# Kernel tuning notes

Measured on AMD Instinct MI355X. Metric: run time of the kernel, lower is better.

Reference implementation:

```python
import jax, jax.numpy as jnp
import numpy as np
import math

D = 256   # d_model / hidden_size
Q = 256   # q_num (query-side nodes)
K = 512   # k_num (key-side nodes)
NEG = -9e15


def _forward(q_enc, k_enc, rel_k, rel_v, k_adj,
             W_glob, b_glob, W_gv0, b_gv0, W_gv1, b_gv1,
             W_gq, b_gq, W_lq, b_lq,
             W_locgate, b_locgate, W_gate, b_gate):
    d = q_enc.shape[-1]
    scale = 1.0 / math.sqrt(d)
    act = jnp.tanh  # activation_func='tanh'

    # --- global sigmoid blending of k_enc with the mean query encoding ---
    q_glob_enc = jnp.mean(q_enc, axis=0)                       # [d]
    k_s = jax.nn.sigmoid((q_glob_enc @ W_glob + b_glob) @ k_enc.T * scale)  # [K]
    k_s = k_s[:, None]                                         # [K,1]
    g_1 = q_glob_enc @ W_gv0 + b_gv0                           # [d]
    k_1 = k_enc @ W_gv1 + b_gv1                                # [K,d]
    k_enc2 = (1.0 - k_s) * k_1 + k_s * g_1                     # [K,d]

    # --- global relation-aware attention over k nodes ---
    q_glob = q_enc @ W_gq + b_gq                               # [Q,d]
    qk_logit = q_glob @ k_enc2.T                               # [Q,K]
    qk_r = jnp.einsum('qd,qkd->qk', q_glob, rel_k)             # [Q,K]
    glob_attn = jax.nn.softmax(act((qk_logit + qk_r) * scale), axis=-1)  # [Q,K]

    # --- local adjacency-masked attention ---
    q_loc = q_enc @ W_lq + b_lq                                # [Q,d]
    qnk_logit = q_loc @ k_enc2.T                               # [Q,K]
    qnk_r = jnp.einsum('qd,qkd->qk', q_loc, rel_k)             # [Q,K]
    loc_attn = act((qnk_logit + qnk_r) * scale)                # [Q,K]
    # loc_weight_rep[q,i,j] = loc_attn[q,j]  (repeat + view in torch)
    mask = (k_adj != 0)[None, :, :]                            # [1,K,K]
    masked = jnp.where(mask, loc_attn[:, None, :], NEG)        # [Q,K,K]
    attn_adj_norm = jax.nn.softmax(masked, axis=-1)            # [Q,K,K]
    k_loc = jnp.einsum('qij,jd->qid', attn_adj_norm, k_enc2)   # [Q,K,d]

    # --- local gate between neighborhood value and self value ---
    # sigmoid(cat([k_loc, k_self]) @ W_locgate + b); k_self is broadcast k_enc2
    Wg1, Wg2 = W_locgate[:d], W_locgate[d:]                    # [d,1] each
    gate_logit = (jnp.einsum('qid,d->qi', k_loc, Wg1[:, 0])
                  + (k_enc2 @ Wg2)[None, :, 0] + b_locgate[0])  # [Q,K]
    loc_gate = jax.nn.sigmoid(gate_logit)[..., None]           # [Q,K,1]
    k_awr = loc_gate * k_loc + (1.0 - loc_gate) * k_enc2[None, :, :]  # [Q,K,d]

    # --- aggregate with global attention + relation values ---
    k_matmul = jnp.einsum('qk,qkd->qd', glob_attn, k_awr)      # [Q,d]
    k_r_matmul = jnp.einsum('qk,qkd->qd', glob_attn, rel_v)    # [Q,d]
    q_enc_new = k_matmul + k_r_matmul                          # [Q,d]

    # --- residual gate ---
    Wq1, Wq2 = W_gate[:d], W_gate[d:]
    gate = jax.nn.sigmoid(q_enc_new @ Wq1 + q_enc @ Wq2 + b_gate)  # [Q,1]
    h = gate * q_enc_new + (1.0 - gate) * q_enc                # [Q,d]
    return h


def setup_inputs() -> dict:
    key = jax.random.key(0)
    ks = jax.random.split(key, 16)
    def w(k, shape):
        return jax.random.normal(k, shape, jnp.float32) * 0.02
    return {
        'q_enc': jax.random.normal(ks[0], (Q, D), jnp.float32),
        'k_enc': jax.random.normal(ks[1], (K, D), jnp.float32),
        'rel_k': jax.random.normal(ks[2], (Q, K, D), jnp.float32) * 0.1,
        'rel_v': jax.random.normal(ks[3], (Q, K, D), jnp.float32) * 0.1,
        'k_adj': jax.random.randint(ks[4], (K, K), 0, 2, jnp.int64) if jax.config.jax_enable_x64 else jax.random.randint(ks[4], (K, K), 0, 2, jnp.int32),
        'W_glob': w(ks[5], (D, D)), 'b_glob': jnp.zeros((D,), jnp.float32),
        'W_gv0': w(ks[6], (D, D)), 'b_gv0': jnp.zeros((D,), jnp.float32),
        'W_gv1': w(ks[7], (D, D)), 'b_gv1': jnp.zeros((D,), jnp.float32),
        'W_gq': w(ks[8], (D, D)), 'b_gq': jnp.zeros((D,), jnp.float32),
        'W_lq': w(ks[9], (D, D)), 'b_lq': jnp.zeros((D,), jnp.float32),
        'W_locgate': w(ks[10], (2 * D, 1)), 'b_locgate': jnp.zeros((1,), jnp.float32),
        'W_gate': w(ks[11], (2 * D, 1)), 'b_gate': jnp.zeros((1,), jnp.float32),
    }


def reference(q_enc, k_enc, rel_k, rel_v, k_adj,
              W_glob, b_glob, W_gv0, b_gv0, W_gv1, b_gv1,
              W_gq, b_gq, W_lq, b_lq,
              W_locgate, b_locgate, W_gate, b_gate):
    return _forward(q_enc, k_enc, rel_k, rel_v, k_adj,
                    W_glob, b_glob, W_gv0, b_gv0, W_gv1, b_gv1,
                    W_gq, b_gq, W_lq, b_lq,
                    W_locgate, b_locgate, W_gate, b_gate)
```

## Files before the change

### kernel.cpp

```cpp
#include <hip/hip_runtime.h>
#include <math.h>

#define QN 256
#define KN 512
#define DN 256
#define SCALE 0.0625f

typedef __attribute__((ext_vector_type(8))) short short8v;
typedef __attribute__((ext_vector_type(4))) float f32x4;

__device__ __forceinline__ float sigf(float x){ return 1.0f/(1.0f+expf(-x)); }

__device__ __forceinline__ unsigned short f2bf(float x){
  unsigned u = __float_as_uint(x);
  unsigned r = (u + 0x7FFFu + ((u >> 16) & 1u)) >> 16;
  return (unsigned short)r;
}

__device__ __forceinline__ short8v ld8(const unsigned short* p){
  ushort4 a = *(const ushort4*)p;
  ushort4 b = *(const ushort4*)(p + 16);
  short8v r;
  r[0]=(short)a.x; r[1]=(short)a.y; r[2]=(short)a.z; r[3]=(short)a.w;
  r[4]=(short)b.x; r[5]=(short)b.y; r[6]=(short)b.z; r[7]=(short)b.w;
  return r;
}

__device__ __forceinline__ float wave_red(float v){
  #pragma unroll
  for (int off = 32; off; off >>= 1) v += __shfl_down(v, off);
  return v;
}

__global__ void kA2(const float* __restrict__ q_enc,
                    const float* __restrict__ W_glob, const float* __restrict__ W_gv0,
                    float* __restrict__ party0, float* __restrict__ party1){
  __shared__ float sm[256][9];
  __shared__ float qm[8];
  int b = blockIdx.x, t = threadIdx.x;
  int j0 = b*8;
  float4 lo = *(const float4*)(q_enc + (size_t)t*DN + j0);
  float4 hi = *(const float4*)(q_enc + (size_t)t*DN + j0 + 4);
  sm[t][0]=lo.x; sm[t][1]=lo.y; sm[t][2]=lo.z; sm[t][3]=lo.w;
  sm[t][4]=hi.x; sm[t][5]=hi.y; sm[t][6]=hi.z; sm[t][7]=hi.w;
  __syncthreads();
  #pragma unroll
  for (int s = 128; s > 0; s >>= 1){
    if (t < s){
      #pragma unroll
      for (int j = 0; j < 8; ++j) sm[t][j] += sm[t+s][j];
    }
    __syncthreads();
  }
  if (t < 8) qm[t] = sm[0][t] * (1.0f/QN);
  __syncthreads();
  float a0 = 0.f, a1 = 0.f;
  #pragma unroll
  for (int j = 0; j < 8; ++j){
    float s = qm[j];
    a0 = fmaf(s, W_glob[(size_t)(j0+j)*DN + t], a0);
    a1 = fmaf(s, W_gv0[(size_t)(j0+j)*DN + t], a1);
  }
  party0[b*256 + t] = a0; party1[b*256 + t] = a1;
}

__global__ void k23(const float* __restrict__ k_enc,
                    const float* __restrict__ W_gv1, const float* __restrict__ b_gv1,
                    const float* __restrict__ party0, const float* __restrict__ party1,
                    const float* __restrict__ b_glob, const float* __restrict__ b_gv0,
                    const float* __restrict__ W_locgate,
                    float* __restrict__ k_enc2, float* __restrict__ cvec,
                    float* __restrict__ gl2,
                    const float* __restrict__ q_enc,
                    const float* __restrict__ W_gq, const float* __restrict__ b_gq,
                    const float* __restrict__ W_lq, const float* __restrict__ b_lq,
                    float* __restrict__ q_glob, float* __restrict__ q_loc,
                    const int* __restrict__ kadj, unsigned short* __restrict__ mbf){
  __shared__ float sh1[256];
  __shared__ float red8[8];
  int bid = blockIdx.x, t = threadIdx.x;
  int w = t >> 6, lane = t & 63;
  int gid = bid*256 + t;
  if (gid < 65536){
    int4 v = ((const int4*)kadj)[gid];
    ushort4 o;
    o.x = v.x ? 0x3F80 : 0; o.y = v.y ? 0x3F80 : 0;
    o.z = v.z ? 0x3F80 : 0; o.w = v.w ? 0x3F80 : 0;
    ((ushort4*)mbf)[gid] = o;
  }
  if (bid < 512){
    int k = bid;
    float tg = b_glob[t], g1v = b_gv0[t];
    #pragma unroll 8
    for (int b2 = 0; b2 < 32; ++b2){
      tg  += party0[b2*256 + t];
      g1v += party1[b2*256 + t];
    }
    float kv = k_enc[(size_t)k*DN + t];
    sh1[t] = kv;
    float part = wave_red(kv * tg);
    if (lane == 0) red8[w] = part;
    __syncthreads();
    float dot = red8[0] + red8[1] + red8[2] + red8[3];
    float ks = sigf(dot * SCALE);
    float acc = b_gv1[t];
    #pragma unroll 8
    for (int j = 0; j < DN; ++j) acc = fmaf(sh1[j], W_gv1[(size_t)j*DN + t], acc);
    float v = (1.f - ks)*acc + ks*g1v;
    k_enc2[(size_t)k*DN + t] = v;
    float pc = wave_red(v * W_locgate[t]);
    float pg = wave_red(v * W_locgate[DN + t]);
    __syncthreads();
    if (lane == 0){ red8[w] = pc; red8[4 + w] = pg; }
    __syncthreads();
    if (t == 0) cvec[k] = red8[0] + red8[1] + red8[2] + red8[3];
    if (t == 1) gl2[k]  = red8[4] + red8[5] + red8[6] + red8[7];
  } else {
    int q = bid - 512;
    sh1[t] = q_enc[(size_t)q*DN + t];
    __syncthreads();
    float a = b_gq[t], b = b_lq[t];
    #pragma unroll 8
    for (int j = 0; j < DN; ++j){
      float s = sh1[j];
      a = fmaf(s, W_gq[(size_t)j*DN + t], a);
      b = fmaf(s, W_lq[(size_t)j*DN + t], b);
    }
    q_glob[(size_t)q*DN + t] = a; q_loc[(size_t)q*DN + t] = b;
  }
}

__global__ void kb2(const float* __restrict__ rel_k,
                    const float* __restrict__ q_glob, const float* __restrict__ q_loc,
                    const float* __restrict__ ke2, const float* __restrict__ cvec,
                    float* __restrict__ exs, float* __restrict__ ev,
                    unsigned short* __restrict__ ebf, unsigned short* __restrict__ ecbf){
  int t = threadIdx.x;
  int wv = t >> 6, lane = t & 63;
  int g = lane >> 4, l16 = lane & 15;
  int b = blockIdx.x;
  int q = b >> 5;
  int k = (b & 31)*16 + wv*4 + g;
  float p1 = 0.f, p2 = 0.f, p3 = 0.f, p4 = 0.f;
  #pragma unroll
  for (int it = 0; it < 4; ++it){
    int d = it*64 + l16*4;
    f32x4 x  = __builtin_nontemporal_load((const f32x4*)(rel_k + ((size_t)q*KN + k)*DN + d));
    float4 a  = *(const float4*)(q_glob + (size_t)q*DN + d);
    float4 bb = *(const float4*)(q_loc  + (size_t)q*DN + d);
    float4 c  = *(const float4*)(ke2    + (size_t)k*DN + d);
    p1 += x[0]*a.x + x[1]*a.y + x[2]*a.z + x[3]*a.w;
    p2 += x[0]*bb.x + x[1]*bb.y + x[2]*bb.z + x[3]*bb.w;
    p3 += c.x*a.x + c.y*a.y + c.z*a.z + c.w*a.w;
    p4 += c.x*bb.x + c.y*bb.y + c.z*bb.z + c.w*bb.w;
  }
  #pragma unroll
  for (int off = 8; off; off >>= 1){
    p1 += __shfl_down(p1, off); p2 += __shfl_down(p2, off);
    p3 += __shfl_down(p3, off); p4 += __shfl_down(p4, off);
  }
  if (l16 == 0){
    size_t idx = (size_t)q*KN + k;
    exs[idx] = expf(tanhf((p1 + p3)*SCALE));
    float evv = expf(tanhf((p2 + p4)*SCALE));
    ev[idx] = evv;
    ebf[idx] = f2bf(evv);
    ecbf[idx] = f2bf(evv * cvec[k]);
  }
}

__global__ __launch_bounds__(256) void kcA2m(const unsigned short* __restrict__ ebf,
                                             const unsigned short* __restrict__ ecbf,
                                             const unsigned short* __restrict__ mbf,
                                             const float* __restrict__ exs,
                                             const float* __restrict__ gl2,
                                             const float* __restrict__ blg_p,
                                             unsigned short* __restrict__ wvbf,
                                             float* __restrict__ v2){
  __shared__ unsigned short Ae[16*520];
  __shared__ unsigned short Ac[16*520];
  __shared__ unsigned short Bm[64*520];
  int t = threadIdx.x;
  int i0 = blockIdx.x*64, q0 = blockIdx.y*16;
  #pragma unroll
  for (int it = 0; it < 4; ++it){
    int c = t + 256*it; int row = c >> 6, col = (c & 63)*8;
    *(uint4*)&Ae[row*520 + col] = *(const uint4*)&ebf[(size_t)(q0+row)*KN + col];
    *(uint4*)&Ac[row*520 + col] = *(const uint4*)&ecbf[(size_t)(q0+row)*KN + col];
  }
  #pragma unroll
  for (int it = 0; it < 16; ++it){
    int c = t + 256*it; int row = c >> 6, col = (c & 63)*8;
    *(uint4*)&Bm[row*520 + col] = *(const uint4*)&mbf[(size_t)(i0+row)*KN + col];
  }
  __syncthreads();
  int w = t >> 6, l = t & 63;
  int g16 = l >> 4, l16 = l & 15;
  f32x4 aS = {0.f,0.f,0.f,0.f}, aN = {0.f,0.f,0.f,0.f};
  const unsigned short* pe = &Ae[l16*520];
  const unsigned short* pc = &Ac[l16*520];
  const unsigned short* pb = &Bm[(16*w + l16)*520];
  #pragma unroll
  for (int kk = 0; kk < 16; ++kk){
    int k0 = kk*32 + 4*g16;
    short8v fa = ld8(pe + k0);
    short8v fc = ld8(pc + k0);
    short8v fb = ld8(pb + k0);
    aS = __builtin_amdgcn_mfma_f32_16x16x32_bf16(fa, fb, aS, 0, 0, 0);
    aN = __builtin_amdgcn_mfma_f32_16x16x32_bf16(fc, fb, aN, 0, 0, 0);
  }
  float blg = blg_p[0];
  int i = i0 + 16*w + l16;
  float gli = gl2[i];
  #pragma unroll
  for (int r = 0; r < 4; ++r){
    int q = q0 + 4*g16 + r;
    size_t idx = (size_t)q*KN + i;
    float s = aS[r], n = aN[r];
    float lgv = sigf(n/s + gli + blg);
    float ex = exs[idx];
    wvbf[idx] = f2bf(ex*lgv/s);
    v2[idx] = ex*(1.f - lgv);
  }
}

__global__ __launch_bounds__(256) void kcC2m(const unsigned short* __restrict__ wvbf,
                                             const unsigned short* __restrict__ mbf,
                                             const float* __restrict__ ev,
                                             const float* __restrict__ v2,
                                             float* __restrict__ coef){
  __shared__ unsigned short Aw[16*520];
  __shared__ unsigned short Bm2[512*72];
  int t = threadIdx.x;
  int j0 = blockIdx.x*64, q0 = blockIdx.y*16;
  #pragma unroll
  for (int it = 0; it < 4; ++it){
    int c = t + 256*it; int row = c >> 6, col = (c & 63)*8;
    *(uint4*)&Aw[row*520 + col] = *(const uint4*)&wvbf[(size_t)(q0+row)*KN + col];
  }
  #pragma unroll
  for (int it = 0; it < 16; ++it){
    int c = t + 256*it; int row = c >> 3, col = (c & 7)*8;
    *(uint4*)&Bm2[row*72 + col] = *(const uint4*)&mbf[(size_t)row*KN + j0 + col];
  }
  __syncthreads();
  int w = t >> 6, l = t & 63;
  int g16 = l >> 4, l16 = l & 15;
  f32x4 aU = {0.f,0.f,0.f,0.f};
  const unsigned short* pa = &Aw[l16*520];
  int nn = 16*w + l16;
  #pragma unroll
  for (int kk = 0; kk < 16; ++kk){
    int k0 = kk*32 + 4*g16;
    short8v fa = ld8(pa + k0);
    short8v fb;
    #pragma unroll
    for (int e = 0; e < 4; ++e){
      fb[e]   = (short)Bm2[(k0+e)*72 + nn];
      fb[4+e] = (short)Bm2[(k0+16+e)*72 + nn];
    }
    aU = __builtin_amdgcn_mfma_f32_16x16x32_bf16(fa, fb, aU, 0, 0, 0);
  }
  int j = j0 + nn;
  #pragma unroll
  for (int r = 0; r < 4; ++r){
    int q = q0 + 4*g16 + r;
    size_t idx = (size_t)q*KN + j;
    coef[idx] = aU[r]*ev[idx] + v2[idx];
  }
}

__global__ __launch_bounds__(512) void kDE(const float* __restrict__ relv,
                                           const float* __restrict__ ke2,
                                           const float* __restrict__ exs,
                                           const float* __restrict__ coef,
                                           const float* __restrict__ q_enc,
                                           const float* __restrict__ W_gate,
                                           const float* __restrict__ b_gate,
                                           float* __restrict__ out){
  __shared__ float red[512];
  __shared__ float4 pacc[8][64];
  int q = blockIdx.x, t = threadIdx.x, w = t >> 6, lane = t & 63;
  red[t] = exs[(size_t)q*KN + t];
  __syncthreads();
  #pragma unroll
  for (int s = 256; s > 0; s >>= 1){
    if (t < s) red[t] += red[t+s];
    __syncthreads();
  }
  float invs = 1.0f / red[0];
  float4 acc = make_float4(0.f,0.f,0.f,0.f);
  int kbase = w*64;
  #pragma unroll 8
  for (int kk = 0; kk < 64; ++kk){
    int k = kbase + kk;
    float gk = exs[(size_t)q*KN + k];
    float ck = coef[(size_t)q*KN + k];
    f32x4 xv = __builtin_nontemporal_load((const f32x4*)(relv + ((size_t)q*KN + k)*DN) + lane);
    float4 kv = ((const float4*)(ke2 + (size_t)k*DN))[lane];
    acc.x = fmaf(gk, xv[0], fmaf(ck, kv.x, acc.x));
    acc.y = fmaf(gk, xv[1], fmaf(ck, kv.y, acc.y));
    acc.z = fmaf(gk, xv[2], fmaf(ck, kv.z, acc.z));
    acc.w = fmaf(gk, xv[3], fmaf(ck, kv.w, acc.w));
  }
  pacc[w][lane] = acc;
  __syncthreads();
  if (t < 64){
    float4 r = pacc[0][t];
    #pragma unroll
    for (int w2 = 1; w2 < 8; ++w2){
      float4 p = pacc[w2][t];
      r.x += p.x; r.y += p.y; r.z += p.z; r.w += p.w;
    }
    r.x *= invs; r.y *= invs; r.z *= invs; r.w *= invs;
    float4 qe = ((const float4*)(q_enc + (size_t)q*DN))[t];
    float4 w1 = ((const float4*)(W_gate))[t];
    float4 w2v = ((const float4*)(W_gate + DN))[t];
    float pd = r.x*w1.x + r.y*w1.y + r.z*w1.z + r.w*w1.w
             + qe.x*w2v.x + qe.y*w2v.y + qe.z*w2v.z + qe.w*w2v.w;
    #pragma unroll
    for (int off = 32; off; off >>= 1) pd += __shfl_down(pd, off);
    float gate = sigf(__shfl(pd, 0) + b_gate[0]);
    float4 h;
    h.x = gate*r.x + (1.f-gate)*qe.x;
    h.y = gate*r.y + (1.f-gate)*qe.y;
    h.z = gate*r.z + (1.f-gate)*qe.z;
    h.w = gate*r.w + (1.f-gate)*qe.w;
    ((float4*)(out + (size_t)q*DN))[t] = h;
  }
}

extern "C" void kernel_launch(void* const* d_in, const int* in_sizes, int n_in,
                              void* d_out, int out_size, void* d_ws, size_t ws_size,
                              hipStream_t stream){
  const float* q_enc     = (const float*)d_in[0];
  const float* k_enc     = (const float*)d_in[1];
  const float* rel_k     = (const float*)d_in[2];
  const float* rel_v     = (const float*)d_in[3];
  const int*   k_adj     = (const int*)  d_in[4];
  const float* W_glob    = (const float*)d_in[5];
  const float* b_glob    = (const float*)d_in[6];
  const float* W_gv0     = (const float*)d_in[7];
  const float* b_gv0     = (const float*)d_in[8];
  const float* W_gv1     = (const float*)d_in[9];
  const float* b_gv1     = (const float*)d_in[10];
  const float* W_gq      = (const float*)d_in[11];
  const float* b_gq      = (const float*)d_in[12];
  const float* W_lq      = (const float*)d_in[13];
  const float* b_lq      = (const float*)d_in[14];
  const float* W_locgate = (const float*)d_in[15];
  const float* b_locgate = (const float*)d_in[16];
  const float* W_gate    = (const float*)d_in[17];
  const float* b_gate    = (const float*)d_in[18];
  float* out = (float*)d_out;

  float* ws = (float*)d_ws;
  float* party0   = ws;
  float* party1   = party0 + 8192;
  float* k_enc2   = party1 + 8192;
  float* cvec     = k_enc2 + 131072;
  float* gl2      = cvec + 512;
  float* q_glob   = gl2 + 512;
  float* q_loc    = q_glob + 65536;
  float* exs      = q_loc + 65536;
  float* evb      = exs + 131072;
  float* v2       = evb + 131072;
  float* coef     = v2 + 131072;
  unsigned short* mbf  = (unsigned short*)(coef + 131072);
  unsigned short* ebf  = mbf + 262144;
  unsigned short* ecbf = ebf + 131072;
  unsigned short* wvbf = ecbf + 131072;

  kA2<<<32, 256, 0, stream>>>(q_enc, W_glob, W_gv0, party0, party1);
  k23<<<768, 256, 0, stream>>>(k_enc, W_gv1, b_gv1, party0, party1, b_glob, b_gv0,
                               W_locgate, k_enc2, cvec, gl2,
                               q_enc, W_gq, b_gq, W_lq, b_lq, q_glob, q_loc,
                               k_adj, mbf);
  kb2<<<8192, 256, 0, stream>>>(rel_k, q_glob, q_loc, k_enc2, cvec,
                                exs, evb, ebf, ecbf);
  kcA2m<<<dim3(8, 16), 256, 0, stream>>>(ebf, ecbf, mbf, exs, gl2, b_locgate, wvbf, v2);
  kcC2m<<<dim3(8, 16), 256, 0, stream>>>(wvbf, mbf, evb, v2, coef);
  kDE<<<256, 512, 0, stream>>>(rel_v, k_enc2, exs, coef, q_enc, W_gate, b_gate, out);
}
```

Baseline: 91.38 us.

## Batch 8 rows per block in projection kernel, move mask conversion, widen kDE

The k_enc2 and q projection kernel now computes 8 rows per block, so each weight element read from global memory is reused across 8 rows instead of 1. The grid shrinks from 768 to 96 blocks, and the reductions move to shared-memory trees. The adjacency-to-bf16 mask conversion moves into kA2. kDE now runs 1024 threads per query, each wave covering 32 keys, to raise parallelism in the rel_v streaming pass. The risks are low occupancy with only 96 blocks and more register pressure from the 8-wide accumulators.

Result: slower. 113.5 us (+24.2%).

```diff
diff --git a/kernel.cpp b/kernel.cpp
--- a/kernel.cpp
+++ b/kernel.cpp
@@ -26,19 +26,23 @@
   return r;
 }
 
-__device__ __forceinline__ float wave_red(float v){
-  #pragma unroll
-  for (int off = 32; off; off >>= 1) v += __shfl_down(v, off);
-  return v;
-}
-
 __global__ void kA2(const float* __restrict__ q_enc,
                     const float* __restrict__ W_glob, const float* __restrict__ W_gv0,
-                    float* __restrict__ party0, float* __restrict__ party1){
+                    float* __restrict__ party0, float* __restrict__ party1,
+                    const int* __restrict__ kadj, unsigned short* __restrict__ mbf){
   __shared__ float sm[256][9];
   __shared__ float qm[8];
   int b = blockIdx.x, t = threadIdx.x;
   int j0 = b*8;
+  #pragma unroll
+  for (int i = 0; i < 8; ++i){
+    int gi = b*2048 + i*256 + t;
+    int4 v = ((const int4*)kadj)[gi];
+    ushort4 o;
+    o.x = v.x ? 0x3F80 : 0; o.y = v.y ? 0x3F80 : 0;
+    o.z = v.z ? 0x3F80 : 0; o.w = v.w ? 0x3F80 : 0;
+    ((ushort4*)mbf)[gi] = o;
+  }
   float4 lo = *(const float4*)(q_enc + (size_t)t*DN + j0);
   float4 hi = *(const float4*)(q_enc + (size_t)t*DN + j0 + 4);
   sm[t][0]=lo.x; sm[t][1]=lo.y; sm[t][2]=lo.z; sm[t][3]=lo.w;
@@ -64,7 +68,7 @@
   party0[b*256 + t] = a0; party1[b*256 + t] = a1;
 }
 
-__global__ void k23(const float* __restrict__ k_enc,
+__global__ __launch_bounds__(256) void k23(const float* __restrict__ k_enc,
                     const float* __restrict__ W_gv1, const float* __restrict__ b_gv1,
                     const float* __restrict__ party0, const float* __restrict__ party1,
                     const float* __restrict__ b_glob, const float* __restrict__ b_gv0,
@@ -74,59 +78,96 @@
                     const float* __restrict__ q_enc,
                     const float* __restrict__ W_gq, const float* __restrict__ b_gq,
                     const float* __restrict__ W_lq, const float* __restrict__ b_lq,
-                    float* __restrict__ q_glob, float* __restrict__ q_loc,
-                    const int* __restrict__ kadj, unsigned short* __restrict__ mbf){
-  __shared__ float sh1[256];
-  __shared__ float red8[8];
+                    float* __restrict__ q_glob, float* __restrict__ q_loc){
+  __shared__ float sh[8][256];
+  __shared__ float2 sred[256][9];
   int bid = blockIdx.x, t = threadIdx.x;
-  int w = t >> 6, lane = t & 63;
-  int gid = bid*256 + t;
-  if (gid < 65536){
-    int4 v = ((const int4*)kadj)[gid];
-    ushort4 o;
-    o.x = v.x ? 0x3F80 : 0; o.y = v.y ? 0x3F80 : 0;
-    o.z = v.z ? 0x3F80 : 0; o.w = v.w ? 0x3F80 : 0;
-    ((ushort4*)mbf)[gid] = o;
-  }
-  if (bid < 512){
-    int k = bid;
+  if (bid < 64){
+    int k0 = bid*8;
     float tg = b_glob[t], g1v = b_gv0[t];
     #pragma unroll 8
     for (int b2 = 0; b2 < 32; ++b2){
       tg  += party0[b2*256 + t];
       g1v += party1[b2*256 + t];
     }
-    float kv = k_enc[(size_t)k*DN + t];
-    sh1[t] = kv;
-    float part = wave_red(kv * tg);
-    if (lane == 0) red8[w] = part;
-    __syncthreads();
-    float dot = red8[0] + red8[1] + red8[2] + red8[3];
-    float ks = sigf(dot * SCALE);
-    float acc = b_gv1[t];
-    #pragma unroll 8
-    for (int j = 0; j < DN; ++j) acc = fmaf(sh1[j], W_gv1[(size_t)j*DN + t], acc);
-    float v = (1.f - ks)*acc + ks*g1v;
-    k_enc2[(size_t)k*DN + t] = v;
-    float pc = wave_red(v * W_locgate[t]);
-    float pg = wave_red(v * W_locgate[DN + t]);
-    __syncthreads();
-    if (lane == 0){ red8[w] = pc; red8[4 + w] = pg; }
-    __syncthreads();
-    if (t == 0) cvec[k] = red8[0] + red8[1] + red8[2] + red8[3];
-    if (t == 1) gl2[k]  = red8[4] + red8[5] + red8[6] + red8[7];
+    float kv[8];
+    #pragma unroll
+    for (int r = 0; r < 8; ++r){
+      kv[r] = k_enc[(size_t)(k0+r)*DN + t];
+      sh[r][t] = kv[r];
+      sred[t][r].x = kv[r] * tg;
+    }
+    __syncthreads();
+    #pragma unroll
+    for (int s = 128; s > 0; s >>= 1){
+      if (t < s){
+        #pragma unroll
+        for (int r = 0; r < 8; ++r) sred[t][r].x += sred[t+s][r].x;
+      }
+      __syncthreads();
+    }
+    float ks[8];
+    #pragma unroll
+    for (int r = 0; r < 8; ++r) ks[r] = sigf(sred[0][r].x * SCALE);
+    __syncthreads();
+    float bgv = b_gv1[t];
+    float acc[8];
+    #pragma unroll
+    for (int r = 0; r < 8; ++r) acc[r] = bgv;
+    #pragma unroll 4
+    for (int j = 0; j < DN; ++j){
+      float wj = W_gv1[(size_t)j*DN + t];
+      #pragma unroll
+      for (int r = 0; r < 8; ++r) acc[r] = fmaf(sh[r][j], wj, acc[r]);
+    }
+    float wg1 = W_locgate[t], wg2 = W_locgate[DN + t];
+    #pragma unroll
+    for (int r = 0; r < 8; ++r){
+      float v = (1.f - ks[r])*acc[r] + ks[r]*g1v;
+      k_enc2[(size_t)(k0+r)*DN + t] = v;
+      sred[t][r].x = v * wg1;
+      sred[t][r].y = v * wg2;
+    }
+    __syncthreads();
+    #pragma unroll
+    for (int s = 128; s > 0; s >>= 1){
+      if (t < s){
+        #pragma unroll
+        for (int r = 0; r < 8; ++r){
+          sred[t][r].x += sred[t+s][r].x;
+          sred[t][r].y += sred[t+s][r].y;
+        }
+      }
+      __syncthreads();
+    }
+    if (t < 8){
+      cvec[k0 + t] = sred[0][t].x;
+      gl2[k0 + t]  = sred[0][t].y;
+    }
   } else {
-    int q = bid - 512;
-    sh1[t] = q_enc[(size_t)q*DN + t];
-    __syncthreads();
-    float a = b_gq[t], b = b_lq[t];
-    #pragma unroll 8
+    int q0 = (bid - 64)*8;
+    #pragma unroll
+    for (int r = 0; r < 8; ++r) sh[r][t] = q_enc[(size_t)(q0+r)*DN + t];
+    __syncthreads();
+    float ba = b_gq[t], bb = b_lq[t];
+    float aa[8], ab[8];
+    #pragma unroll
+    for (int r = 0; r < 8; ++r){ aa[r] = ba; ab[r] = bb; }
+    #pragma unroll 2
     for (int j = 0; j < DN; ++j){
-      float s = sh1[j];
-      a = fmaf(s, W_gq[(size_t)j*DN + t], a);
-      b = fmaf(s, W_lq[(size_t)j*DN + t], b);
-    }
-    q_glob[(size_t)q*DN + t] = a; q_loc[(size_t)q*DN + t] = b;
+      float wa = W_gq[(size_t)j*DN + t];
+      float wb = W_lq[(size_t)j*DN + t];
+      #pragma unroll
+      for (int r = 0; r < 8; ++r){
+        aa[r] = fmaf(sh[r][j], wa, aa[r]);
+        ab[r] = fmaf(sh[r][j], wb, ab[r]);
+      }
+    }
+    #pragma unroll
+    for (int r = 0; r < 8; ++r){
+      q_glob[(size_t)(q0+r)*DN + t] = aa[r];
+      q_loc[(size_t)(q0+r)*DN + t]  = ab[r];
+    }
   }
 }
 
@@ -270,18 +311,18 @@
   }
 }
 
-__global__ __launch_bounds__(512) void kDE(const float* __restrict__ relv,
-                                           const float* __restrict__ ke2,
-                                           const float* __restrict__ exs,
-                                           const float* __restrict__ coef,
-                                           const float* __restrict__ q_enc,
-                                           const float* __restrict__ W_gate,
-                                           const float* __restrict__ b_gate,
-                                           float* __restrict__ out){
+__global__ __launch_bounds__(1024) void kDE(const float* __restrict__ relv,
+                                            const float* __restrict__ ke2,
+                                            const float* __restrict__ exs,
+                                            const float* __restrict__ coef,
+                                            const float* __restrict__ q_enc,
+                                            const float* __restrict__ W_gate,
+                                            const float* __restrict__ b_gate,
+                                            float* __restrict__ out){
   __shared__ float red[512];
-  __shared__ float4 pacc[8][64];
+  __shared__ float4 pacc[16][64];
   int q = blockIdx.x, t = threadIdx.x, w = t >> 6, lane = t & 63;
-  red[t] = exs[(size_t)q*KN + t];
+  if (t < 512) red[t] = exs[(size_t)q*KN + t];
   __syncthreads();
   #pragma unroll
   for (int s = 256; s > 0; s >>= 1){
@@ -290,9 +331,9 @@
   }
   float invs = 1.0f / red[0];
   float4 acc = make_float4(0.f,0.f,0.f,0.f);
-  int kbase = w*64;
+  int kbase = w*32;
   #pragma unroll 8
-  for (int kk = 0; kk < 64; ++kk){
+  for (int kk = 0; kk < 32; ++kk){
     int k = kbase + kk;
     float gk = exs[(size_t)q*KN + k];
     float ck = coef[(size_t)q*KN + k];
@@ -308,7 +349,7 @@
   if (t < 64){
     float4 r = pacc[0][t];
     #pragma unroll
-    for (int w2 = 1; w2 < 8; ++w2){
+    for (int w2 = 1; w2 < 16; ++w2){
       float4 p = pacc[w2][t];
       r.x += p.x; r.y += p.y; r.z += p.z; r.w += p.w;
     }
@@ -371,14 +412,13 @@
   unsigned short* ecbf = ebf + 131072;
   unsigned short* wvbf = ecbf + 131072;
 
-  kA2<<<32, 256, 0, stream>>>(q_enc, W_glob, W_gv0, party0, party1);
-  k23<<<768, 256, 0, stream>>>(k_enc, W_gv1, b_gv1, party0, party1, b_glob, b_gv0,
-                               W_locgate, k_enc2, cvec, gl2,
-                               q_enc, W_gq, b_gq, W_lq, b_lq, q_glob, q_loc,
-                               k_adj, mbf);
+  kA2<<<32, 256, 0, stream>>>(q_enc, W_glob, W_gv0, party0, party1, k_adj, mbf);
+  k23<<<96, 256, 0, stream>>>(k_enc, W_gv1, b_gv1, party0, party1, b_glob, b_gv0,
+                              W_locgate, k_enc2, cvec, gl2,
+                              q_enc, W_gq, b_gq, W_lq, b_lq, q_glob, q_loc);
   kb2<<<8192, 256, 0, stream>>>(rel_k, q_glob, q_loc, k_enc2, cvec,
                                 exs, evb, ebf, ecbf);
   kcA2m<<<dim3(8, 16), 256, 0, stream>>>(ebf, ecbf, mbf, exs, gl2, b_locgate, wvbf, v2);
   kcC2m<<<dim3(8, 16), 256, 0, stream>>>(wvbf, mbf, evb, v2, coef);
-  kDE<<<256, 512, 0, stream>>>(rel_v, k_enc2, exs, coef, q_enc, W_gate, b_gate, out);
-}
+  kDE<<<256, 1024, 0, stream>>>(rel_v, k_enc2, exs, coef, q_enc, W_gate, b_gate, out);
+}
```
